# Kernel tuning notes

Measured on AMD Instinct MI355X. Metric: run time of the kernel, lower is better.

The kernel has to match this reference:

```python
import jax, jax.numpy as jnp
import numpy as np

N = 50000
E = 1600000
F_IN = 512
H1, C1 = 8, 8          # layer1: 8 heads x 8 channels, concat -> 64
C2 = 40                # layer2: 1 head, num_classes
NEG_SLOPE = 0.2


def setup_inputs() -> dict:
    key = jax.random.key(0)
    ks = jax.random.split(key, 12)
    x = jax.random.normal(ks[0], (N, F_IN), dtype=jnp.float32)
    edge_index = jax.random.randint(ks[1], (2, E), 0, N, dtype=jnp.int32)
    s1 = 1.0 / np.sqrt(F_IN)
    W1 = jax.random.uniform(ks[2], (F_IN, H1 * C1), jnp.float32, -s1, s1)
    att_src1 = jax.random.normal(ks[3], (1, H1, C1), dtype=jnp.float32) * 0.1
    att_dst1 = jax.random.normal(ks[4], (1, H1, C1), dtype=jnp.float32) * 0.1
    b1 = jnp.zeros((H1 * C1,), jnp.float32)
    s2 = 1.0 / np.sqrt(H1 * C1)
    W2 = jax.random.uniform(ks[5], (H1 * C1, C2), jnp.float32, -s2, s2)
    att_src2 = jax.random.normal(ks[6], (1, 1, C2), dtype=jnp.float32) * 0.1
    att_dst2 = jax.random.normal(ks[7], (1, 1, C2), dtype=jnp.float32) * 0.1
    b2 = jnp.zeros((C2,), jnp.float32)
    return {"x": x, "edge_index": edge_index,
            "W1": W1, "att_src1": att_src1, "att_dst1": att_dst1, "b1": b1,
            "W2": W2, "att_src2": att_src2, "att_dst2": att_dst2, "b2": b2}


def gat_conv(x, W, att_src, att_dst, bias, src, dst, heads, out_ch, concat):
    n = x.shape[0]
    h = (x @ W).reshape(n, heads, out_ch)                 # [N,H,C]
    a_src = (h * att_src).sum(-1)                          # [N,H]
    a_dst = (h * att_dst).sum(-1)                          # [N,H]
    logits = jax.nn.leaky_relu(a_src[src] + a_dst[dst], NEG_SLOPE)  # [E,H]
    # segment softmax over incoming edges per destination node
    m = jax.ops.segment_max(logits, dst, num_segments=n)   # [N,H]
    ex = jnp.exp(logits - m[dst])                          # [E,H]
    denom = jax.ops.segment_sum(ex, dst, num_segments=n)   # [N,H]
    w = ex / denom[dst]                                    # [E,H]
    out = jax.ops.segment_sum(h[src] * w[:, :, None], dst, num_segments=n)  # [N,H,C]
    if concat:
        out = out.reshape(n, heads * out_ch)
    else:
        out = out.mean(axis=1)
    return out + bias


def reference(x, edge_index, W1, att_src1, att_dst1, b1, W2, att_src2, att_dst2, b2):
    # add self loops (PyG add_self_loops=True)
    loop = jnp.arange(N, dtype=edge_index.dtype)
    src = jnp.concatenate([edge_index[0], loop])
    dst = jnp.concatenate([edge_index[1], loop])
    # dropout is identity in eval mode
    h = gat_conv(x, W1, att_src1, att_dst1, b1, src, dst, H1, C1, True)
    h = jax.nn.relu(h)
    h = gat_conv(h, W2, att_src2, att_dst2, b2, src, dst, 1, C2, False)
    return jax.nn.log_softmax(h, axis=1)
```

## Files before the change

### kernel.cpp

```cpp
#include <hip/hip_runtime.h>
#include <math.h>

#define NN 50000
#define EE 1600000
#define FIN 512
#define H1N 8
#define C2N 40
#define NEG 0.2f

#define NB 391
#define CAPG 6144
#define PA_ITEMS 4096
#define NITEMS (EE + NN)
#define PA_BLOCKS ((NITEMS + PA_ITEMS - 1) / PA_ITEMS)
#define W1T_BLOCKS 32

typedef __attribute__((ext_vector_type(8))) short bf16x8;
typedef __attribute__((ext_vector_type(4))) float f32x4;

__device__ inline short f2bf(float f) {
  unsigned int u = __float_as_uint(f);
  u += 0x7FFFu + ((u >> 16) & 1u);
  return (short)(u >> 16);
}
__device__ inline unsigned int pack2bf(float lo, float hi) {
  return (unsigned int)(unsigned short)f2bf(lo) | ((unsigned int)(unsigned short)f2bf(hi) << 16);
}
__device__ inline float bflo(unsigned int v) { return __uint_as_float(v << 16); }
__device__ inline float bfhi(unsigned int v) { return __uint_as_float(v & 0xFFFF0000u); }

__global__ __launch_bounds__(256) void passA_kernel(const int* __restrict__ ei,
    int* __restrict__ bucket_cnt, unsigned int* __restrict__ bucket_glob,
    const float* __restrict__ W1, short* __restrict__ WT) {
  int t = threadIdx.x;
  if (blockIdx.x >= PA_BLOCKS) {
    int base = (blockIdx.x - PA_BLOCKS) * 1024 + t * 4;
#pragma unroll
    for (int j = 0; j < 4; ++j) {
      int i = base + j;
      int n = i >> 9, k = i & 511;
      WT[i] = f2bf(W1[k * 64 + n]);
    }
    return;
  }
  __shared__ int hist[NB];
  __shared__ int prefix[NB];
  __shared__ int cursor[NB];
  __shared__ int gbase[NB];
  __shared__ int scA[512], scB[512];
  __shared__ unsigned int staging[PA_ITEMS];
  int i0 = blockIdx.x * PA_ITEMS;
  int count = NITEMS - i0; if (count > PA_ITEMS) count = PA_ITEMS;

  for (int b = t; b < NB; b += 256) hist[b] = 0;
  __syncthreads();
  for (int j = t; j < count; j += 256) {
    int e = i0 + j;
    int dst = (e < EE) ? ei[EE + e] : (e - EE);
    atomicAdd(&hist[dst >> 7], 1);
  }
  __syncthreads();
  scA[t]       = (t < NB) ? hist[t] : 0;
  scA[t + 256] = (t + 256 < NB) ? hist[t + 256] : 0;
  __syncthreads();
  {
    int* pa = scA; int* pb = scB;
    for (int off = 1; off < 512; off <<= 1) {
      pb[t]       = pa[t]       + (t >= off ? pa[t - off] : 0);
      pb[t + 256] = pa[t + 256] + (t + 256 >= off ? pa[t + 256 - off] : 0);
      __syncthreads();
      int* tmp = pa; pa = pb; pb = tmp;
    }
    for (int b = t; b < NB; b += 256) {
      int ex = pa[b] - hist[b];
      prefix[b] = ex;
      cursor[b] = ex;
      if (hist[b] > 0) gbase[b] = atomicAdd(&bucket_cnt[b], hist[b]);
    }
  }
  __syncthreads();
  for (int j = t; j < count; j += 256) {
    int e = i0 + j;
    int src, dst;
    if (e < EE) { src = ei[e]; dst = ei[EE + e]; }
    else        { src = e - EE; dst = src; }
    int b = dst >> 7;
    unsigned int v = (unsigned int)src | ((unsigned int)(dst & 127) << 16)
                   | ((unsigned int)b << 23);
    int lp = atomicAdd(&cursor[b], 1);
    staging[lp] = v;
  }
  __syncthreads();
  for (int j = t; j < count; j += 256) {
    unsigned int v = staging[j];
    int b = (int)(v >> 23);
    int gpos = b * CAPG + gbase[b] + (j - prefix[b]);
    bucket_glob[gpos] = v;
  }
}

__global__ __launch_bounds__(512) void scan_buckets(const int* __restrict__ bucket_cnt,
    int* __restrict__ bucket_base, int* __restrict__ row_ptr_last) {
  __shared__ int scA[512], scB[512];
  int t = threadIdx.x;
  int v = (t < NB) ? bucket_cnt[t] : 0;
  scA[t] = v;
  __syncthreads();
  int* pa = scA; int* pb = scB;
  for (int off = 1; off < 512; off <<= 1) {
    pb[t] = pa[t] + (t >= off ? pa[t - off] : 0);
    __syncthreads();
    int* tmp = pa; pa = pb; pb = tmp;
  }
  if (t < NB) bucket_base[t] = pa[t] - v;
  if (t == NB - 1) *row_ptr_last = pa[t];
}

#define CAPB 6144
__global__ __launch_bounds__(256) void passB_kernel(const unsigned int* __restrict__ bucket_glob,
    const int* __restrict__ bucket_cnt, const int* __restrict__ bucket_base,
    int* __restrict__ row_ptr, int* __restrict__ col) {
  __shared__ int hist[128], pre[128], cur[128];
  __shared__ int scA[128], scB[128];
  __shared__ int sorted[CAPB];
  int b = blockIdx.x, t = threadIdx.x;
  int cnt = bucket_cnt[b];
  int base = bucket_base[b];
  const unsigned int* in = bucket_glob + (size_t)b * CAPG;
  if (t < 128) hist[t] = 0;
  __syncthreads();
  for (int j = t; j < cnt; j += 256) {
    int dl = (int)((in[j] >> 16) & 127u);
    atomicAdd(&hist[dl], 1);
  }
  __syncthreads();
  if (t < 128) scA[t] = hist[t];
  __syncthreads();
  {
    int* pa = scA; int* pb = scB;
    for (int off = 1; off < 128; off <<= 1) {
      if (t < 128) pb[t] = pa[t] + (t >= off ? pa[t - off] : 0);
      __syncthreads();
      int* tmp = pa; pa = pb; pb = tmp;
    }
    if (t < 128) {
      int ex = pa[t] - hist[t];
      pre[t] = ex;
      cur[t] = ex;
      int d = b * 128 + t;
      if (d < NN) row_ptr[d] = base + ex;
    }
  }
  __syncthreads();
  for (int j = t; j < cnt; j += 256) {
    unsigned int v = in[j];
    int dl = (int)((v >> 16) & 127u);
    int lp = atomicAdd(&cur[dl], 1);
    sorted[lp] = (int)(v & 0xFFFFu);
  }
  __syncthreads();
  for (int j = t; j < cnt; j += 256) col[base + j] = sorted[j];
}


#define XS_STRIDE 136
#define HS_STRIDE 68
__global__ __launch_bounds__(256) void gemm1_kernel(const float* __restrict__ x,
    const short* __restrict__ WT, unsigned short* __restrict__ h1b,
    const float* __restrict__ att_src, const float* __restrict__ att_dst,
    float* __restrict__ asrc, float* __restrict__ adst) {
  __shared__ char smem[64 * XS_STRIDE * 2];
  short* xs = (short*)smem;
  float* hsf = (float*)smem;
  int t = threadIdx.x;
  int wave = t >> 6, lane = t & 63;
  int quad = lane >> 4, m = lane & 15;
  int row0 = blockIdx.x * 64;
  f32x4 acc[4] = {{0.f,0.f,0.f,0.f},{0.f,0.f,0.f,0.f},{0.f,0.f,0.f,0.f},{0.f,0.f,0.f,0.f}};
  for (int kc = 0; kc < 4; ++kc) {
    int k0 = kc * 128;
    __syncthreads();
#pragma unroll
    for (int jj = 0; jj < 8; ++jj) {
      int idx = jj * 256 + t;
      int row = idx >> 5, kq = idx & 31;
      int rr = row0 + row; if (rr >= NN) rr = NN - 1;
      float4 v = *(const float4*)(x + (size_t)rr * FIN + k0 + kq * 4);
      short4 s;
      s.x = f2bf(v.x); s.y = f2bf(v.y); s.z = f2bf(v.z); s.w = f2bf(v.w);
      *(short4*)&xs[row * XS_STRIDE + kq * 4] = s;
    }
    __syncthreads();
#pragma unroll
    for (int ks = 0; ks < 4; ++ks) {
      bf16x8 a = *(bf16x8*)&xs[(wave * 16 + m) * XS_STRIDE + ks * 32 + quad * 8];
#pragma unroll
      for (int tl = 0; tl < 4; ++tl) {
        bf16x8 b = *(const bf16x8*)(WT + (size_t)(tl * 16 + m) * 512 + k0 + ks * 32 + quad * 8);
        acc[tl] = __builtin_amdgcn_mfma_f32_16x16x32_bf16(a, b, acc[tl], 0, 0, 0);
      }
    }
  }
  __syncthreads();
  int rl0 = wave * 16 + quad * 4;
#pragma unroll
  for (int tl = 0; tl < 4; ++tl) {
#pragma unroll
    for (int r = 0; r < 4; ++r) {
      int rr = row0 + rl0 + r;
      if (rr < NN) h1b[(size_t)rr * 64 + tl * 16 + m] = (unsigned short)f2bf(acc[tl][r]);
      hsf[(rl0 + r) * HS_STRIDE + tl * 16 + m] = acc[tl][r];
    }
  }
  __syncthreads();
#pragma unroll
  for (int p = 0; p < 2; ++p) {
    int idx = p * 256 + t;
    int rl = idx >> 3, h = idx & 7;
    int rr = row0 + rl;
    if (rr < NN) {
      const float* hv = &hsf[rl * HS_STRIDE + h * 8];
      const float* as = att_src + h * 8;
      const float* ad = att_dst + h * 8;
      float s = 0.f, dd = 0.f;
#pragma unroll
      for (int c = 0; c < 8; ++c) { s = fmaf(hv[c], as[c], s); dd = fmaf(hv[c], ad[c], dd); }
      asrc[rr * 8 + h] = s;
      adst[rr * 8 + h] = dd;
    }
  }
}


__global__ __launch_bounds__(256) void l1_edge_kernel(const int* __restrict__ row_ptr,
    const int* __restrict__ col, const unsigned int* __restrict__ h1b,
    const float* __restrict__ asrc, const float* __restrict__ adst,
    const float* __restrict__ b1, const float* __restrict__ W2,
    const float* __restrict__ att_src2, const float* __restrict__ att_dst2,
    unsigned int* __restrict__ gb, float* __restrict__ asrc2, float* __restrict__ adst2) {
  __shared__ float w2s[64 * C2N];
  __shared__ float hs[4][64];
  __shared__ float gs[4][48];
  int t = threadIdx.x;
  for (int i = t; i < 64 * C2N; i += 256) w2s[i] = W2[i];
  __syncthreads();
  int wave = t >> 6, lane = t & 63;
  int g = lane & 7, j = lane >> 3;
#pragma unroll 1
  for (int iter = 0; iter < 4; ++iter) {
    int d = blockIdx.x * 16 + iter * 4 + wave;
    if (d >= NN) break;
    int start = row_ptr[d], end = row_ptr[d + 1];
    float adst_h = adst[d * 8 + g];
    float acc[8] = {0.f,0.f,0.f,0.f,0.f,0.f,0.f,0.f};
    float den = 0.f;
    for (int e = start; e < end; e += 16) {
      int i1 = e + j, i2 = e + 8 + j;
      int k1 = i1 < end ? i1 : end - 1;
      int k2 = i2 < end ? i2 : end - 1;
      int s1 = col[k1], s2 = col[k2];
      float av1 = asrc[s1 * 8 + g];
      float av2 = asrc[s2 * 8 + g];
      uint4 hv1 = *(const uint4*)(h1b + (size_t)s1 * 32 + g * 4);
      uint4 hv2 = *(const uint4*)(h1b + (size_t)s2 * 32 + g * 4);
      float a1 = av1 + adst_h, a2 = av2 + adst_h;
      float lg1 = fmaxf(a1, NEG * a1);
      float lg2 = fmaxf(a2, NEG * a2);
      float ex1 = (i1 < end) ? __expf(lg1) : 0.f;
      float ex2 = (i2 < end) ? __expf(lg2) : 0.f;
      den += ex1 + ex2;
      acc[0] = fmaf(ex1, bflo(hv1.x), acc[0]); acc[0] = fmaf(ex2, bflo(hv2.x), acc[0]);
      acc[1] = fmaf(ex1, bfhi(hv1.x), acc[1]); acc[1] = fmaf(ex2, bfhi(hv2.x), acc[1]);
      acc[2] = fmaf(ex1, bflo(hv1.y), acc[2]); acc[2] = fmaf(ex2, bflo(hv2.y), acc[2]);
      acc[3] = fmaf(ex1, bfhi(hv1.y), acc[3]); acc[3] = fmaf(ex2, bfhi(hv2.y), acc[3]);
      acc[4] = fmaf(ex1, bflo(hv1.z), acc[4]); acc[4] = fmaf(ex2, bflo(hv2.z), acc[4]);
      acc[5] = fmaf(ex1, bfhi(hv1.z), acc[5]); acc[5] = fmaf(ex2, bfhi(hv2.z), acc[5]);
      acc[6] = fmaf(ex1, bflo(hv1.w), acc[6]); acc[6] = fmaf(ex2, bflo(hv2.w), acc[6]);
      acc[7] = fmaf(ex1, bfhi(hv1.w), acc[7]); acc[7] = fmaf(ex2, bfhi(hv2.w), acc[7]);
    }
#pragma unroll
    for (int off = 8; off <= 32; off <<= 1) {
      den += __shfl_xor(den, off);
#pragma unroll
      for (int c = 0; c < 8; ++c) acc[c] += __shfl_xor(acc[c], off);
    }
    float inv = 1.f / den;
    if (j == 0) {
      float4 b1a = *(const float4*)(b1 + g * 8);
      float4 b1b = *(const float4*)(b1 + g * 8 + 4);
      float4 h0, h1v;
      h0.x = fmaxf(fmaf(acc[0], inv, b1a.x), 0.f);
      h0.y = fmaxf(fmaf(acc[1], inv, b1a.y), 0.f);
      h0.z = fmaxf(fmaf(acc[2], inv, b1a.z), 0.f);
      h0.w = fmaxf(fmaf(acc[3], inv, b1a.w), 0.f);
      h1v.x = fmaxf(fmaf(acc[4], inv, b1b.x), 0.f);
      h1v.y = fmaxf(fmaf(acc[5], inv, b1b.y), 0.f);
      h1v.z = fmaxf(fmaf(acc[6], inv, b1b.z), 0.f);
      h1v.w = fmaxf(fmaf(acc[7], inv, b1b.w), 0.f);
      *(float4*)&hs[wave][g * 8]     = h0;
      *(float4*)&hs[wave][g * 8 + 4] = h1v;
    }
    int c = lane;
    float gacc = 0.f;
    if (c < C2N) {
#pragma unroll
      for (int k = 0; k < 64; ++k) gacc = fmaf(hs[wave][k], w2s[k * C2N + c], gacc);
    }
    float asv = (c < C2N) ? gacc * att_src2[c] : 0.f;
    float adv = (c < C2N) ? gacc * att_dst2[c] : 0.f;
#pragma unroll
    for (int off = 32; off >= 1; off >>= 1) {
      asv += __shfl_xor(asv, off);
      adv += __shfl_xor(adv, off);
    }
    if (lane == 0) { asrc2[d] = asv; adst2[d] = adv; }
    if (c < C2N) gs[wave][c] = gacc;
    if (lane < 20) gb[(size_t)d * 20 + lane] = pack2bf(gs[wave][2 * lane], gs[wave][2 * lane + 1]);
  }
}


__global__ __launch_bounds__(256) void l2_edge_kernel(const int* __restrict__ row_ptr,
    const int* __restrict__ col, const unsigned int* __restrict__ gb,
    const float* __restrict__ asrc2, const float* __restrict__ adst2,
    const float* __restrict__ b2, float* __restrict__ out) {
  int t = threadIdx.x;
  int d = (blockIdx.x * 256 + t) >> 6;
  if (d >= NN) return;
  int lane = t & 63;
  int g = lane & 7, j = lane >> 3;
  int gq = (g < 5) ? g : 4;
  bool act = g < 5;
  int start = row_ptr[d], end = row_ptr[d + 1];
  float adst_d = adst2[d];
  float acc[8] = {0.f,0.f,0.f,0.f,0.f,0.f,0.f,0.f};
  float den = 0.f;
  for (int e = start; e < end; e += 16) {
    int i1 = e + j, i2 = e + 8 + j;
    int k1 = i1 < end ? i1 : end - 1;
    int k2 = i2 < end ? i2 : end - 1;
    int s1 = col[k1], s2 = col[k2];
    float av1 = asrc2[s1], av2 = asrc2[s2];
    uint4 g1 = *(const uint4*)(gb + (size_t)s1 * 20 + gq * 4);
    uint4 g2 = *(const uint4*)(gb + (size_t)s2 * 20 + gq * 4);
    float a1 = av1 + adst_d, a2 = av2 + adst_d;
    float lg1 = fmaxf(a1, NEG * a1);
    float lg2 = fmaxf(a2, NEG * a2);
    float ex1 = (i1 < end) ? __expf(lg1) : 0.f;
    float ex2 = (i2 < end) ? __expf(lg2) : 0.f;
    den += ex1 + ex2;
    acc[0] = fmaf(ex1, bflo(g1.x), acc[0]); acc[0] = fmaf(ex2, bflo(g2.x), acc[0]);
    acc[1] = fmaf(ex1, bfhi(g1.x), acc[1]); acc[1] = fmaf(ex2, bfhi(g2.x), acc[1]);
    acc[2] = fmaf(ex1, bflo(g1.y), acc[2]); acc[2] = fmaf(ex2, bflo(g2.y), acc[2]);
    acc[3] = fmaf(ex1, bfhi(g1.y), acc[3]); acc[3] = fmaf(ex2, bfhi(g2.y), acc[3]);
    acc[4] = fmaf(ex1, bflo(g1.z), acc[4]); acc[4] = fmaf(ex2, bflo(g2.z), acc[4]);
    acc[5] = fmaf(ex1, bfhi(g1.z), acc[5]); acc[5] = fmaf(ex2, bfhi(g2.z), acc[5]);
    acc[6] = fmaf(ex1, bflo(g1.w), acc[6]); acc[6] = fmaf(ex2, bflo(g2.w), acc[6]);
    acc[7] = fmaf(ex1, bfhi(g1.w), acc[7]); acc[7] = fmaf(ex2, bfhi(g2.w), acc[7]);
  }
#pragma unroll
  for (int off = 8; off <= 32; off <<= 1) {
    den += __shfl_xor(den, off);
#pragma unroll
    for (int c = 0; c < 8; ++c) acc[c] += __shfl_xor(acc[c], off);
  }
  float inv = 1.f / den;
  float4 b2a = *(const float4*)(b2 + gq * 8);
  float4 b2b = *(const float4*)(b2 + gq * 8 + 4);
  float o[8];
  o[0] = fmaf(acc[0], inv, b2a.x); o[1] = fmaf(acc[1], inv, b2a.y);
  o[2] = fmaf(acc[2], inv, b2a.z); o[3] = fmaf(acc[3], inv, b2a.w);
  o[4] = fmaf(acc[4], inv, b2b.x); o[5] = fmaf(acc[5], inv, b2b.y);
  o[6] = fmaf(acc[6], inv, b2b.z); o[7] = fmaf(acc[7], inv, b2b.w);
  float m = -INFINITY;
  if (act) {
#pragma unroll
    for (int i = 0; i < 8; ++i) m = fmaxf(m, o[i]);
  }
#pragma unroll
  for (int off = 1; off <= 4; off <<= 1) m = fmaxf(m, __shfl_xor(m, off));
  float es = 0.f;
  if (act) {
#pragma unroll
    for (int i = 0; i < 8; ++i) es += __expf(o[i] - m);
  }
#pragma unroll
  for (int off = 1; off <= 4; off <<= 1) es += __shfl_xor(es, off);
  float mls = m + logf(es);
  if (act && j == 0) {
    float4 r0 = make_float4(o[0] - mls, o[1] - mls, o[2] - mls, o[3] - mls);
    float4 r1 = make_float4(o[4] - mls, o[5] - mls, o[6] - mls, o[7] - mls);
    *(float4*)(out + (size_t)d * C2N + g * 8)     = r0;
    *(float4*)(out + (size_t)d * C2N + g * 8 + 4) = r1;
  }
}


extern "C" void kernel_launch(void* const* d_in, const int* in_sizes, int n_in,
                              void* d_out, int out_size, void* d_ws, size_t ws_size,
                              hipStream_t stream) {
  const float* x        = (const float*)d_in[0];
  const int*   ei       = (const int*)d_in[1];
  const float* W1       = (const float*)d_in[2];
  const float* att_src1 = (const float*)d_in[3];
  const float* att_dst1 = (const float*)d_in[4];
  const float* b1       = (const float*)d_in[5];
  const float* W2       = (const float*)d_in[6];
  const float* att_src2 = (const float*)d_in[7];
  const float* att_dst2 = (const float*)d_in[8];
  const float* b2       = (const float*)d_in[9];
  float* out = (float*)d_out;

  char* ws = (char*)d_ws;
  size_t off = 0;
  auto alloc = [&](size_t n_elem) {
    void* p = ws + off;
    off = (off + n_elem * 4 + 255) & ~(size_t)255;
    return p;
  };
  unsigned int* h1b = (unsigned int*)alloc((size_t)NN * 32);
  unsigned int* gb  = (unsigned int*)alloc((size_t)NN * 20 + 16);
  unsigned int* bucket_glob = (unsigned int*)alloc((size_t)NB * CAPG);
  float* asrc1 = (float*)alloc((size_t)NN * 8);
  float* adst1 = (float*)alloc((size_t)NN * 8);
  float* asrc2 = (float*)alloc(NN);
  float* adst2 = (float*)alloc(NN);
  int* row_ptr = (int*)alloc(NN + 1);
  int* colv    = (int*)alloc(EE + NN);
  int* bucket_cnt  = (int*)alloc(NB);
  int* bucket_base = (int*)alloc(NB);
  short* w1t   = (short*)alloc(64 * 512 / 2);

  hipMemsetAsync(bucket_cnt, 0, NB * 4, stream);
  passA_kernel<<<PA_BLOCKS + W1T_BLOCKS, 256, 0, stream>>>(ei, bucket_cnt, bucket_glob, W1, w1t);
  scan_buckets<<<1, 512, 0, stream>>>(bucket_cnt, bucket_base, row_ptr + NN);
  passB_kernel<<<NB, 256, 0, stream>>>(bucket_glob, bucket_cnt, bucket_base, row_ptr, colv);

  gemm1_kernel<<<(NN + 63) / 64, 256, 0, stream>>>(x, w1t, (unsigned short*)h1b,
                                                   att_src1, att_dst1, asrc1, adst1);
  l1_edge_kernel<<<(NN + 15) / 16, 256, 0, stream>>>(row_ptr, colv, h1b, asrc1, adst1,
                                                     b1, W2, att_src2, att_dst2,
                                                     gb, asrc2, adst2);
  l2_edge_kernel<<<(NN * 64 + 255) / 256, 256, 0, stream>>>(row_ptr, colv, gb, asrc2, adst2, b2, out);
}
```

Measured before the change: 329.7 us.

## Fuse bucket scan into passB, cache dst in registers, skip empty second edge loads

```diff
diff --git a/kernel.cpp b/kernel.cpp
--- a/kernel.cpp
+++ b/kernel.cpp
@@ -54,10 +54,16 @@
 
   for (int b = t; b < NB; b += 256) hist[b] = 0;
   __syncthreads();
-  for (int j = t; j < count; j += 256) {
-    int e = i0 + j;
-    int dst = (e < EE) ? ei[EE + e] : (e - EE);
-    atomicAdd(&hist[dst >> 7], 1);
+  int dstv[16];
+#pragma unroll
+  for (int ii = 0; ii < 16; ++ii) {
+    int jj = ii * 256 + t;
+    if (jj < count) {
+      int e = i0 + jj;
+      int dst = (e < EE) ? ei[EE + e] : (e - EE);
+      dstv[ii] = dst;
+      atomicAdd(&hist[dst >> 7], 1);
+    }
   }
   __syncthreads();
   scA[t]       = (t < NB) ? hist[t] : 0;
@@ -79,16 +85,19 @@
     }
   }
   __syncthreads();
-  for (int j = t; j < count; j += 256) {
-    int e = i0 + j;
-    int src, dst;
-    if (e < EE) { src = ei[e]; dst = ei[EE + e]; }
-    else        { src = e - EE; dst = src; }
-    int b = dst >> 7;
-    unsigned int v = (unsigned int)src | ((unsigned int)(dst & 127) << 16)
-                   | ((unsigned int)b << 23);
-    int lp = atomicAdd(&cursor[b], 1);
-    staging[lp] = v;
+#pragma unroll
+  for (int ii = 0; ii < 16; ++ii) {
+    int jj = ii * 256 + t;
+    if (jj < count) {
+      int e = i0 + jj;
+      int src = (e < EE) ? ei[e] : (e - EE);
+      int dst = dstv[ii];
+      int b = dst >> 7;
+      unsigned int v = (unsigned int)src | ((unsigned int)(dst & 127) << 16)
+                     | ((unsigned int)b << 23);
+      int lp = atomicAdd(&cursor[b], 1);
+      staging[lp] = v;
+    }
   }
   __syncthreads();
   for (int j = t; j < count; j += 256) {
@@ -99,33 +108,27 @@
   }
 }
 
-__global__ __launch_bounds__(512) void scan_buckets(const int* __restrict__ bucket_cnt,
-    int* __restrict__ bucket_base, int* __restrict__ row_ptr_last) {
+#define CAPB 6144
+__global__ __launch_bounds__(256) void passB_kernel(const unsigned int* __restrict__ bucket_glob,
+    const int* __restrict__ bucket_cnt, int* __restrict__ row_ptr, int* __restrict__ col) {
   __shared__ int scA[512], scB[512];
-  int t = threadIdx.x;
-  int v = (t < NB) ? bucket_cnt[t] : 0;
-  scA[t] = v;
+  __shared__ int hist[128], cur[128];
+  __shared__ int sorted[CAPB];
+  int b = blockIdx.x, t = threadIdx.x;
+  scA[t]       = (t < NB) ? bucket_cnt[t] : 0;
+  scA[t + 256] = (t + 256 < NB) ? bucket_cnt[t + 256] : 0;
   __syncthreads();
   int* pa = scA; int* pb = scB;
   for (int off = 1; off < 512; off <<= 1) {
-    pb[t] = pa[t] + (t >= off ? pa[t - off] : 0);
+    pb[t]       = pa[t]       + (t >= off ? pa[t - off] : 0);
+    pb[t + 256] = pa[t + 256] + (t + 256 >= off ? pa[t + 256 - off] : 0);
     __syncthreads();
     int* tmp = pa; pa = pb; pb = tmp;
   }
-  if (t < NB) bucket_base[t] = pa[t] - v;
-  if (t == NB - 1) *row_ptr_last = pa[t];
-}
-
-#define CAPB 6144
-__global__ __launch_bounds__(256) void passB_kernel(const unsigned int* __restrict__ bucket_glob,
-    const int* __restrict__ bucket_cnt, const int* __restrict__ bucket_base,
-    int* __restrict__ row_ptr, int* __restrict__ col) {
-  __shared__ int hist[128], pre[128], cur[128];
-  __shared__ int scA[128], scB[128];
-  __shared__ int sorted[CAPB];
-  int b = blockIdx.x, t = threadIdx.x;
   int cnt = bucket_cnt[b];
-  int base = bucket_base[b];
+  int base = pa[b] - cnt;
+  if (b == 0 && t == 0) row_ptr[NN] = pa[NB - 1];
+  __syncthreads();
   const unsigned int* in = bucket_glob + (size_t)b * CAPG;
   if (t < 128) hist[t] = 0;
   __syncthreads();
@@ -137,15 +140,14 @@
   if (t < 128) scA[t] = hist[t];
   __syncthreads();
   {
-    int* pa = scA; int* pb = scB;
+    int* qa = scA; int* qb = scB;
     for (int off = 1; off < 128; off <<= 1) {
-      if (t < 128) pb[t] = pa[t] + (t >= off ? pa[t - off] : 0);
+      if (t < 128) qb[t] = qa[t] + (t >= off ? qa[t - off] : 0);
       __syncthreads();
-      int* tmp = pa; pa = pb; pb = tmp;
+      int* tmp = qa; qa = qb; qb = tmp;
     }
     if (t < 128) {
-      int ex = pa[t] - hist[t];
-      pre[t] = ex;
+      int ex = qa[t] - hist[t];
       cur[t] = ex;
       int d = b * 128 + t;
       if (d < NN) row_ptr[d] = base + ex;
@@ -255,19 +257,29 @@
     float acc[8] = {0.f,0.f,0.f,0.f,0.f,0.f,0.f,0.f};
     float den = 0.f;
     for (int e = start; e < end; e += 16) {
-      int i1 = e + j, i2 = e + 8 + j;
+      bool two = (e + 8) < end;
+      int i1 = e + j;
       int k1 = i1 < end ? i1 : end - 1;
-      int k2 = i2 < end ? i2 : end - 1;
-      int s1 = col[k1], s2 = col[k2];
+      int s1 = col[k1];
+      int s2 = 0;
+      if (two) {
+        int i2 = e + 8 + j;
+        int k2 = i2 < end ? i2 : end - 1;
+        s2 = col[k2];
+      }
       float av1 = asrc[s1 * 8 + g];
-      float av2 = asrc[s2 * 8 + g];
       uint4 hv1 = *(const uint4*)(h1b + (size_t)s1 * 32 + g * 4);
-      uint4 hv2 = *(const uint4*)(h1b + (size_t)s2 * 32 + g * 4);
+      float av2 = 0.f;
+      uint4 hv2 = make_uint4(0u, 0u, 0u, 0u);
+      if (two) {
+        av2 = asrc[s2 * 8 + g];
+        hv2 = *(const uint4*)(h1b + (size_t)s2 * 32 + g * 4);
+      }
       float a1 = av1 + adst_h, a2 = av2 + adst_h;
       float lg1 = fmaxf(a1, NEG * a1);
       float lg2 = fmaxf(a2, NEG * a2);
       float ex1 = (i1 < end) ? __expf(lg1) : 0.f;
-      float ex2 = (i2 < end) ? __expf(lg2) : 0.f;
+      float ex2 = (two && (e + 8 + j) < end) ? __expf(lg2) : 0.f;
       den += ex1 + ex2;
       acc[0] = fmaf(ex1, bflo(hv1.x), acc[0]); acc[0] = fmaf(ex2, bflo(hv2.x), acc[0]);
       acc[1] = fmaf(ex1, bfhi(hv1.x), acc[1]); acc[1] = fmaf(ex2, bfhi(hv2.x), acc[1]);
@@ -336,18 +348,29 @@
   float acc[8] = {0.f,0.f,0.f,0.f,0.f,0.f,0.f,0.f};
   float den = 0.f;
   for (int e = start; e < end; e += 16) {
-    int i1 = e + j, i2 = e + 8 + j;
+    bool two = (e + 8) < end;
+    int i1 = e + j;
     int k1 = i1 < end ? i1 : end - 1;
-    int k2 = i2 < end ? i2 : end - 1;
-    int s1 = col[k1], s2 = col[k2];
-    float av1 = asrc2[s1], av2 = asrc2[s2];
+    int s1 = col[k1];
+    int s2 = 0;
+    if (two) {
+      int i2 = e + 8 + j;
+      int k2 = i2 < end ? i2 : end - 1;
+      s2 = col[k2];
+    }
+    float av1 = asrc2[s1];
     uint4 g1 = *(const uint4*)(gb + (size_t)s1 * 20 + gq * 4);
-    uint4 g2 = *(const uint4*)(gb + (size_t)s2 * 20 + gq * 4);
+    float av2 = 0.f;
+    uint4 g2 = make_uint4(0u, 0u, 0u, 0u);
+    if (two) {
+      av2 = asrc2[s2];
+      g2 = *(const uint4*)(gb + (size_t)s2 * 20 + gq * 4);
+    }
     float a1 = av1 + adst_d, a2 = av2 + adst_d;
     float lg1 = fmaxf(a1, NEG * a1);
     float lg2 = fmaxf(a2, NEG * a2);
     float ex1 = (i1 < end) ? __expf(lg1) : 0.f;
-    float ex2 = (i2 < end) ? __expf(lg2) : 0.f;
+    float ex2 = (two && (e + 8 + j) < end) ? __expf(lg2) : 0.f;
     den += ex1 + ex2;
     acc[0] = fmaf(ex1, bflo(g1.x), acc[0]); acc[0] = fmaf(ex2, bflo(g2.x), acc[0]);
     acc[1] = fmaf(ex1, bfhi(g1.x), acc[1]); acc[1] = fmaf(ex2, bfhi(g2.x), acc[1]);
@@ -428,13 +451,11 @@
   int* row_ptr = (int*)alloc(NN + 1);
   int* colv    = (int*)alloc(EE + NN);
   int* bucket_cnt  = (int*)alloc(NB);
-  int* bucket_base = (int*)alloc(NB);
   short* w1t   = (short*)alloc(64 * 512 / 2);
 
   hipMemsetAsync(bucket_cnt, 0, NB * 4, stream);
   passA_kernel<<<PA_BLOCKS + W1T_BLOCKS, 256, 0, stream>>>(ei, bucket_cnt, bucket_glob, W1, w1t);
-  scan_buckets<<<1, 512, 0, stream>>>(bucket_cnt, bucket_base, row_ptr + NN);
-  passB_kernel<<<NB, 256, 0, stream>>>(bucket_glob, bucket_cnt, bucket_base, row_ptr, colv);
+  passB_kernel<<<NB, 256, 0, stream>>>(bucket_glob, bucket_cnt, row_ptr, colv);
 
   gemm1_kernel<<<(NN + 63) / 64, 256, 0, stream>>>(x, w1t, (unsigned short*)h1b,
                                                    att_src1, att_dst1, asrc1, adst1);
```

New measurement: 326.8 us. No clear change (-0.9%).
